# Kernel optimization log

Hardware: AMD Instinct MI355X
Metric: run time of the kernel (lower is better)

Reference implementation:

```python
import jax, jax.numpy as jnp
import numpy as np

B, S, D = 8, 2048, 1024
NEG = -1000000000.0  # float32 masking constant from original code


def setup_inputs() -> dict:
    key = jax.random.key(0)
    kq, kk, kv, km = jax.random.split(key, 4)
    q = jax.random.normal(kq, (B, S, D), dtype=jnp.float32)
    k = jax.random.normal(kk, (B, S, D), dtype=jnp.float32)
    v = jax.random.normal(kv, (B, S, D), dtype=jnp.float32)
    mask = (jax.random.uniform(km, (B, 1, S)) < 0.1).astype(jnp.float32)
    return {"q": q, "k": k, "v": v, "mask": mask}


def reference(q, k, v, mask):
    scale = jnp.asarray(D ** -0.5, dtype=q.dtype)
    # [B,S,S] = q @ k^T, scaled
    logits = jnp.einsum("bqd,bkd->bqk", q, k) * scale
    logits = logits + mask * NEG  # mask broadcasts over query axis
    attn = jax.nn.softmax(logits, axis=-1)
    return jnp.einsum("bqk,bkd->bqd", attn, v)
```

## Files before the change

kernel.cpp:

```cpp
#include <hip/hip_runtime.h>
#include <hip/hip_bf16.h>

#define NB 8
#define SS 2048
#define DDIM 1024

typedef __attribute__((ext_vector_type(8))) short bf16x8;
typedef __attribute__((ext_vector_type(4))) float f32x4;

__device__ inline void gload_lds16(const void* g, void* l) {
  __builtin_amdgcn_global_load_lds(
      (const __attribute__((address_space(1))) void*)g,
      (__attribute__((address_space(3))) void*)l, 16, 0, 0);
}

__device__ inline ushort f2bf(float f) {
  union { float f; unsigned int u; } v;
  v.f = f;
  unsigned int u = v.u;
  unsigned int r = (u + 0x7FFFu + ((u >> 16) & 1u)) >> 16;
  return (ushort)r;
}

__device__ inline unsigned int pack2(float a, float b) {
  return (unsigned int)f2bf(a) | ((unsigned int)f2bf(b) << 16);
}

__global__ void init_zero(float* __restrict__ p, int n) {
  int i = blockIdx.x * 256 + threadIdx.x;
  if (i < n) p[i] = 0.f;
}

__global__ void conv_bf16_qk(const float* __restrict__ qin,
                             const float* __restrict__ kin,
                             ushort* __restrict__ qout,
                             ushort* __restrict__ kout, int n8) {
  int i = blockIdx.x * 256 + threadIdx.x;
  if (i >= n8) return;
  const float* in = blockIdx.y ? kin : qin;
  ushort* out = blockIdx.y ? kout : qout;
  const float4* p = (const float4*)in + (size_t)i * 2;
  float4 a = p[0], b = p[1];
  uint4 o;
  o.x = pack2(a.x, a.y);
  o.y = pack2(a.z, a.w);
  o.z = pack2(b.x, b.y);
  o.w = pack2(b.z, b.w);
  ((uint4*)out)[i] = o;
}

__global__ void conv_transpose_v(const float* __restrict__ V,
                                 ushort* __restrict__ VT) {
  __shared__ ushort tile[64][65];
  const int b = blockIdx.z;
  const int k0 = blockIdx.x * 64;
  const int d0 = blockIdx.y * 64;
  const float* Vb = V + (size_t)b * SS * DDIM;
  ushort* VTb = VT + (size_t)b * DDIM * SS;
  const int t = threadIdx.x;
#pragma unroll
  for (int i = 0; i < 4; i++) {
    int j = i * 256 + t;
    int r = j >> 4, cg = j & 15;
    float4 f = *(const float4*)(Vb + (size_t)(k0 + r) * DDIM + d0 + cg * 4);
    tile[r][cg * 4 + 0] = f2bf(f.x);
    tile[r][cg * 4 + 1] = f2bf(f.y);
    tile[r][cg * 4 + 2] = f2bf(f.z);
    tile[r][cg * 4 + 3] = f2bf(f.w);
  }
  __syncthreads();
#pragma unroll
  for (int i = 0; i < 2; i++) {
    int j = i * 256 + t;
    int r = j >> 3, cg = j & 7;
    ushort u[8];
#pragma unroll
    for (int u8 = 0; u8 < 8; u8++) u[u8] = tile[cg * 8 + u8][r];
    *(uint4*)(VTb + (size_t)(d0 + r) * SS + k0 + cg * 8) = *(uint4*)u;
  }
}

#define MFMA16(mh, nh)                                                        \
  _Pragma("unroll") for (int ks = 0; ks < 2; ks++)                            \
  _Pragma("unroll") for (int mi = 0; mi < 4; mi++)                            \
  _Pragma("unroll") for (int ni = 0; ni < 2; ni++)                            \
      acc[mh][mi][nh][ni] = __builtin_amdgcn_mfma_f32_16x16x32_bf16(          \
          af[mi][ks], bf[ni][ks], acc[mh][mi][nh][ni], 0, 0, 0);

#define BARRIER() asm volatile("s_barrier" ::: "memory")

#define PHASE(mh, nh)                                                         \
  BARRIER();                                                                  \
  __builtin_amdgcn_s_setprio(1);                                              \
  MFMA16(mh, nh);                                                             \
  __builtin_amdgcn_s_setprio(0);

#define VMW(n) asm volatile("s_waitcnt vmcnt(" #n ")" ::: "memory")
#define ENDP() BARRIER()

#define RD_A(d, h)                                                            \
  _Pragma("unroll") for (int mi = 0; mi < 4; mi++) {                          \
    const char* _p = ldsc + (d) * 65536 + (h) * 16384 + aoff[mi];             \
    af[mi][0] = *(const bf16x8*)(_p + koff0);                                 \
    af[mi][1] = *(const bf16x8*)(_p + koff1);                                 \
  }

#define RD_B(d, h)                                                            \
  _Pragma("unroll") for (int ni = 0; ni < 2; ni++) {                          \
    const char* _p = ldsc + (d) * 65536 + 32768 + (h) * 16384 + boff[ni];     \
    bf[ni][0] = *(const bf16x8*)(_p + koff0);                                 \
    bf[ni][1] = *(const bf16x8*)(_p + koff1);                                 \
  }

#define STAGE(dbuf, isB, h, kt_)                                              \
  do {                                                                        \
    const ushort* _s = (isB) ? Bb : Ab;                                       \
    const int _t0 = (isB) ? tileN : tileM;                                    \
    char* _lb = ldsc + (dbuf) * 65536 + (isB) * 32768 + (h) * 16384;          \
    gload_lds16(_s + (size_t)(_t0 + (h) * 128 + r0) * K + (kt_) * 64 + c8,    \
                _lb + ol0);                                                   \
    gload_lds16(_s + (size_t)(_t0 + (h) * 128 + r1) * K + (kt_) * 64 + c8,    \
                _lb + ol1);                                                   \
  } while (0)

template <bool EXPEPI, typename OutT>
__global__ __launch_bounds__(512, 2) void gemm_bt(
    const ushort* __restrict__ A, const ushort* __restrict__ Bm,
    OutT* __restrict__ C, const float* __restrict__ maskp,
    float* __restrict__ rowsum, int M, int N, int K, float alpha) {
  __shared__ __attribute__((aligned(128))) char ldsc[131072];
  const int tid = threadIdx.x;
  const int wave = tid >> 6, lane = tid & 63;
  const int quad = lane >> 4, l16 = lane & 15;
  const int wm = wave >> 2, wn = wave & 3;

  const int gx = gridDim.x, gy = gridDim.y;
  const int lin = blockIdx.x + gx * (blockIdx.y + gy * blockIdx.z);
  const int nwg = gx * gy * (int)gridDim.z;
  const int cpx = nwg >> 3;
  const int swz = (lin & 7) * cpx + (lin >> 3);
  const int bz = swz / (gx * gy);
  const int rem = swz - bz * (gx * gy);
  const int by = rem / gx;
  const int bx = rem - by * gx;

  const int b = bz;
  const ushort* Ab = A + (size_t)b * M * K;
  const ushort* Bb = Bm + (size_t)b * N * K;
  const int tileM = by * 256, tileN = bx * 256;

  const int ol0 = wave * 2048 + lane * 16;
  const int ol1 = ol0 + 1024;
  const int r0 = ol0 >> 7;
  const int r1 = r0 + 8;
  const int c8 = (((lane & 7) ^ (r0 & 7)) * 8);

  const int x7 = lane & 7;
  const int koff0 = ((quad) ^ x7) * 16;
  const int koff1 = ((4 + quad) ^ x7) * 16;
  int aoff[4], boff[2];
#pragma unroll
  for (int mi = 0; mi < 4; mi++) aoff[mi] = (wm * 64 + mi * 16 + l16) * 128;
#pragma unroll
  for (int ni = 0; ni < 2; ni++) boff[ni] = (wn * 32 + ni * 16 + l16) * 128;

  f32x4 acc[2][4][2][2];
#pragma unroll
  for (int mh = 0; mh < 2; mh++)
#pragma unroll
    for (int mi = 0; mi < 4; mi++)
#pragma unroll
      for (int nh = 0; nh < 2; nh++)
#pragma unroll
        for (int ni = 0; ni < 2; ni++)
          acc[mh][mi][nh][ni] = (f32x4){0.f, 0.f, 0.f, 0.f};

  bf16x8 af[4][2], bf[2][2];
  const int NKT = K >> 6;

  STAGE(0, 0, 0, 0);
  STAGE(0, 1, 0, 0);
  STAGE(0, 1, 1, 0);
  STAGE(0, 0, 1, 0);
  VMW(4);
  BARRIER();

  for (int kt = 0; kt < NKT - 1; ++kt) {
    const int d = kt & 1, dn = d ^ 1;
    RD_A(d, 0); RD_B(d, 0); STAGE(dn, 0, 0, kt + 1);
    PHASE(0, 0); VMW(4); ENDP();
    RD_B(d, 1);             STAGE(dn, 1, 0, kt + 1);
    PHASE(0, 1); VMW(4); ENDP();
    RD_A(d, 1);             STAGE(dn, 1, 1, kt + 1);
    PHASE(1, 1); ENDP();
    RD_B(d, 0);             STAGE(dn, 0, 1, kt + 1);
    PHASE(1, 0); VMW(4); ENDP();
  }
  {
    const int d = (NKT - 1) & 1;
    RD_A(d, 0); RD_B(d, 0);
    PHASE(0, 0); VMW(2); ENDP();
    RD_B(d, 1);
    PHASE(0, 1); VMW(0); ENDP();
    RD_A(d, 1);
    PHASE(1, 1); ENDP();
    RD_B(d, 0);
    PHASE(1, 0); ENDP();
  }

  OutT* Cb = C + (size_t)b * M * N;
  if (EXPEPI) {
    const float* mb = maskp + (size_t)b * N;
    float mv[2][2];
#pragma unroll
    for (int nh = 0; nh < 2; nh++)
#pragma unroll
      for (int ni = 0; ni < 2; ni++)
        mv[nh][ni] = mb[tileN + nh * 128 + wn * 32 + ni * 16 + l16] * (-1e9f);
#pragma unroll
    for (int mh = 0; mh < 2; mh++)
#pragma unroll
    for (int mi = 0; mi < 4; mi++) {
#pragma unroll
      for (int rr = 0; rr < 4; rr++) {
        const int row = tileM + mh * 128 + wm * 64 + mi * 16 + quad * 4 + rr;
        float s = 0.f;
#pragma unroll
        for (int nh = 0; nh < 2; nh++)
#pragma unroll
        for (int ni = 0; ni < 2; ni++) {
          const int col = tileN + nh * 128 + wn * 32 + ni * 16 + l16;
          float e = __expf(acc[mh][mi][nh][ni][rr] * alpha + mv[nh][ni]);
          ((ushort*)Cb)[(size_t)row * N + col] = f2bf(e);
          s += e;
        }
        s += __shfl_xor(s, 1, 64);
        s += __shfl_xor(s, 2, 64);
        s += __shfl_xor(s, 4, 64);
        s += __shfl_xor(s, 8, 64);
        if (l16 == 0) atomicAdd(&rowsum[(size_t)b * M + row], s);
      }
    }
  } else {
#pragma unroll
    for (int mh = 0; mh < 2; mh++)
#pragma unroll
    for (int mi = 0; mi < 4; mi++) {
      float inv[4];
#pragma unroll
      for (int rr = 0; rr < 4; rr++) {
        const int row = tileM + mh * 128 + wm * 64 + mi * 16 + quad * 4 + rr;
        inv[rr] = 1.0f / rowsum[(size_t)b * M + row];
      }
#pragma unroll
      for (int nh = 0; nh < 2; nh++)
#pragma unroll
      for (int ni = 0; ni < 2; ni++) {
        const int col = tileN + nh * 128 + wn * 32 + ni * 16 + l16;
#pragma unroll
        for (int rr = 0; rr < 4; rr++) {
          const int row = tileM + mh * 128 + wm * 64 + mi * 16 + quad * 4 + rr;
          ((float*)Cb)[(size_t)row * N + col] =
              acc[mh][mi][nh][ni][rr] * alpha * inv[rr];
        }
      }
    }
  }
}

extern "C" void kernel_launch(void* const* d_in, const int* in_sizes, int n_in,
                              void* d_out, int out_size, void* d_ws, size_t ws_size,
                              hipStream_t stream) {
  const float* q = (const float*)d_in[0];
  const float* k = (const float*)d_in[1];
  const float* v = (const float*)d_in[2];
  const float* mask = (const float*)d_in[3];
  float* out = (float*)d_out;

  const size_t pQ = (size_t)SS * DDIM * 2;
  const size_t pP = (size_t)SS * SS * 2;
  const size_t pR = (size_t)SS * 4;

  int gb = 8;
  while (gb > 1 && (size_t)gb * (3 * pQ + pP + pR) > ws_size) gb >>= 1;

  for (int b0 = 0; b0 < NB; b0 += gb) {
    char* w = (char*)d_ws;
    ushort* qb = (ushort*)w;
    ushort* kb = (ushort*)(w + (size_t)gb * pQ);
    ushort* vtb = (ushort*)(w + (size_t)gb * pQ * 2);
    ushort* Sc = (ushort*)(w + (size_t)gb * pQ * 3);
    float* rowsum = (float*)(w + (size_t)gb * (pQ * 3 + pP));

    const float* qg = q + (size_t)b0 * SS * DDIM;
    const float* kg = k + (size_t)b0 * SS * DDIM;
    const float* vg = v + (size_t)b0 * SS * DDIM;
    const float* mg = mask + (size_t)b0 * SS;
    float* og = out + (size_t)b0 * SS * DDIM;

    const int nrs = gb * SS;
    init_zero<<<(nrs + 255) / 256, 256, 0, stream>>>(rowsum, nrs);
    const int n8 = gb * SS * DDIM / 8;
    conv_bf16_qk<<<dim3(n8 / 256, 2), 256, 0, stream>>>(qg, kg, qb, kb, n8);
    conv_transpose_v<<<dim3(SS / 64, DDIM / 64, gb), 256, 0, stream>>>(vg, vtb);
    gemm_bt<true, ushort><<<dim3(SS / 256, SS / 256, gb), 512, 0, stream>>>(
        qb, kb, Sc, mg, rowsum, SS, SS, DDIM, 0.03125f);
    gemm_bt<false, float><<<dim3(DDIM / 256, SS / 256, gb), 512, 0, stream>>>(
        Sc, vtb, og, nullptr, rowsum, SS, DDIM, SS, 1.0f);
  }
}
```

Baseline: 359.5 us.

## Compute softmax row sums with extra MFMAs in the PV GEMM instead of atomics

Removes the atomic row-sum accumulation, the cross-lane shuffles and the rowsum zero-init kernel from the QK^T exp epilogue. The PV GEMM instead gets row sums by multiplying each loaded P fragment against a bf16 ones vector with MFMA. This also normalises with the same bf16-rounded probabilities used in the numerator. The cost is more MFMA work in the second GEMM's inner loop and extra accumulator registers, which under the 512-thread, 2-block launch bound could cause pressure or spills.

```diff
diff --git a/kernel.cpp b/kernel.cpp
--- a/kernel.cpp
+++ b/kernel.cpp
@@ -24,11 +24,6 @@
 
 __device__ inline unsigned int pack2(float a, float b) {
   return (unsigned int)f2bf(a) | ((unsigned int)f2bf(b) << 16);
-}
-
-__global__ void init_zero(float* __restrict__ p, int n) {
-  int i = blockIdx.x * 256 + threadIdx.x;
-  if (i < n) p[i] = 0.f;
 }
 
 __global__ void conv_bf16_qk(const float* __restrict__ qin,
@@ -87,6 +82,16 @@
       acc[mh][mi][nh][ni] = __builtin_amdgcn_mfma_f32_16x16x32_bf16(          \
           af[mi][ks], bf[ni][ks], acc[mh][mi][nh][ni], 0, 0, 0);
 
+#define ROWSUM(mh)                                                            \
+  if constexpr (!EXPEPI) {                                                    \
+    _Pragma("unroll") for (int mi = 0; mi < 4; mi++) {                        \
+      acc1[mh][mi] = __builtin_amdgcn_mfma_f32_16x16x32_bf16(                 \
+          af[mi][0], ones, acc1[mh][mi], 0, 0, 0);                            \
+      acc1[mh][mi] = __builtin_amdgcn_mfma_f32_16x16x32_bf16(                 \
+          af[mi][1], ones, acc1[mh][mi], 0, 0, 0);                            \
+    }                                                                         \
+  }
+
 #define BARRIER() asm volatile("s_barrier" ::: "memory")
 
 #define PHASE(mh, nh)                                                         \
@@ -126,8 +131,8 @@
 template <bool EXPEPI, typename OutT>
 __global__ __launch_bounds__(512, 2) void gemm_bt(
     const ushort* __restrict__ A, const ushort* __restrict__ Bm,
-    OutT* __restrict__ C, const float* __restrict__ maskp,
-    float* __restrict__ rowsum, int M, int N, int K, float alpha) {
+    OutT* __restrict__ C, const float* __restrict__ maskp, int M, int N,
+    int K, float alpha) {
   __shared__ __attribute__((aligned(128))) char ldsc[131072];
   const int tid = threadIdx.x;
   const int wave = tid >> 6, lane = tid & 63;
@@ -175,6 +180,15 @@
         for (int ni = 0; ni < 2; ni++)
           acc[mh][mi][nh][ni] = (f32x4){0.f, 0.f, 0.f, 0.f};
 
+  f32x4 acc1[2][4];
+  bf16x8 ones;
+#pragma unroll
+  for (int mh = 0; mh < 2; mh++)
+#pragma unroll
+    for (int mi = 0; mi < 4; mi++) acc1[mh][mi] = (f32x4){0.f, 0.f, 0.f, 0.f};
+#pragma unroll
+  for (int i = 0; i < 8; i++) ones[i] = (short)0x3F80;
+
   bf16x8 af[4][2], bf[2][2];
   const int NKT = K >> 6;
 
@@ -188,28 +202,28 @@
   for (int kt = 0; kt < NKT - 1; ++kt) {
     const int d = kt & 1, dn = d ^ 1;
     RD_A(d, 0); RD_B(d, 0); STAGE(dn, 0, 0, kt + 1);
-    PHASE(0, 0); VMW(4); ENDP();
+    PHASE(0, 0); ROWSUM(0); VMW(4); ENDP();
     RD_B(d, 1);             STAGE(dn, 1, 0, kt + 1);
     PHASE(0, 1); VMW(4); ENDP();
     RD_A(d, 1);             STAGE(dn, 1, 1, kt + 1);
-    PHASE(1, 1); ENDP();
+    PHASE(1, 1); ROWSUM(1); ENDP();
     RD_B(d, 0);             STAGE(dn, 0, 1, kt + 1);
     PHASE(1, 0); VMW(4); ENDP();
   }
   {
     const int d = (NKT - 1) & 1;
     RD_A(d, 0); RD_B(d, 0);
-    PHASE(0, 0); VMW(2); ENDP();
+    PHASE(0, 0); ROWSUM(0); VMW(2); ENDP();
     RD_B(d, 1);
     PHASE(0, 1); VMW(0); ENDP();
     RD_A(d, 1);
-    PHASE(1, 1); ENDP();
+    PHASE(1, 1); ROWSUM(1); ENDP();
     RD_B(d, 0);
     PHASE(1, 0); ENDP();
   }
 
   OutT* Cb = C + (size_t)b * M * N;
-  if (EXPEPI) {
+  if constexpr (EXPEPI) {
     const float* mb = maskp + (size_t)b * N;
     float mv[2][2];
 #pragma unroll
@@ -224,7 +238,6 @@
 #pragma unroll
       for (int rr = 0; rr < 4; rr++) {
         const int row = tileM + mh * 128 + wm * 64 + mi * 16 + quad * 4 + rr;
-        float s = 0.f;
 #pragma unroll
         for (int nh = 0; nh < 2; nh++)
 #pragma unroll
@@ -232,13 +245,7 @@
           const int col = tileN + nh * 128 + wn * 32 + ni * 16 + l16;
           float e = __expf(acc[mh][mi][nh][ni][rr] * alpha + mv[nh][ni]);
           ((ushort*)Cb)[(size_t)row * N + col] = f2bf(e);
-          s += e;
         }
-        s += __shfl_xor(s, 1, 64);
-        s += __shfl_xor(s, 2, 64);
-        s += __shfl_xor(s, 4, 64);
-        s += __shfl_xor(s, 8, 64);
-        if (l16 == 0) atomicAdd(&rowsum[(size_t)b * M + row], s);
       }
     }
   } else {
@@ -248,10 +255,7 @@
     for (int mi = 0; mi < 4; mi++) {
       float inv[4];
 #pragma unroll
-      for (int rr = 0; rr < 4; rr++) {
-        const int row = tileM + mh * 128 + wm * 64 + mi * 16 + quad * 4 + rr;
-        inv[rr] = 1.0f / rowsum[(size_t)b * M + row];
-      }
+      for (int rr = 0; rr < 4; rr++) inv[rr] = 1.0f / acc1[mh][mi][rr];
 #pragma unroll
       for (int nh = 0; nh < 2; nh++)
 #pragma unroll
@@ -279,10 +283,9 @@
 
   const size_t pQ = (size_t)SS * DDIM * 2;
   const size_t pP = (size_t)SS * SS * 2;
-  const size_t pR = (size_t)SS * 4;
 
   int gb = 8;
-  while (gb > 1 && (size_t)gb * (3 * pQ + pP + pR) > ws_size) gb >>= 1;
+  while (gb > 1 && (size_t)gb * (3 * pQ + pP) > ws_size) gb >>= 1;
 
   for (int b0 = 0; b0 < NB; b0 += gb) {
     char* w = (char*)d_ws;
@@ -290,7 +293,6 @@
     ushort* kb = (ushort*)(w + (size_t)gb * pQ);
     ushort* vtb = (ushort*)(w + (size_t)gb * pQ * 2);
     ushort* Sc = (ushort*)(w + (size_t)gb * pQ * 3);
-    float* rowsum = (float*)(w + (size_t)gb * (pQ * 3 + pP));
 
     const float* qg = q + (size_t)b0 * SS * DDIM;
     const float* kg = k + (size_t)b0 * SS * DDIM;
@@ -298,14 +300,12 @@
     const float* mg = mask + (size_t)b0 * SS;
     float* og = out + (size_t)b0 * SS * DDIM;
 
-    const int nrs = gb * SS;
-    init_zero<<<(nrs + 255) / 256, 256, 0, stream>>>(rowsum, nrs);
     const int n8 = gb * SS * DDIM / 8;
     conv_bf16_qk<<<dim3(n8 / 256, 2), 256, 0, stream>>>(qg, kg, qb, kb, n8);
     conv_transpose_v<<<dim3(SS / 64, DDIM / 64, gb), 256, 0, stream>>>(vg, vtb);
     gemm_bt<true, ushort><<<dim3(SS / 256, SS / 256, gb), 512, 0, stream>>>(
-        qb, kb, Sc, mg, rowsum, SS, SS, DDIM, 0.03125f);
+        qb, kb, Sc, mg, SS, SS, DDIM, 0.03125f);
     gemm_bt<false, float><<<dim3(DDIM / 256, SS / 256, gb), 512, 0, stream>>>(
-        Sc, vtb, og, nullptr, rowsum, SS, DDIM, SS, 1.0f);
-  }
-}
+        Sc, vtb, og, nullptr, SS, DDIM, SS, 1.0f);
+  }
+}
```

After: 352.0 us. 2.1% less time.
